# Optimization experiments

Hardware: AMD Instinct MI355X
Metric: run time of the kernel (lower is better)

Reference implementation:

```python
import jax, jax.numpy as jnp
import numpy as np

B, T, D, H, HD, F, L = 4, 2048, 768, 8, 96, 2048, 2
EPS = 1e-6


def _l2norm(x):
    return x * jax.lax.rsqrt(jnp.sum(x * x, -1, keepdims=True) + EPS)


def _layernorm(x, w, b):
    m = jnp.mean(x, -1, keepdims=True)
    v = jnp.var(x, -1, keepdims=True)
    return (x - m) * jax.lax.rsqrt(v + 1e-5) * w + b


def setup_inputs() -> dict:
    key = jax.random.key(0)
    ks = iter(jax.random.split(key, 40))
    def p(shape, scale=0.02):
        return jax.random.normal(next(ks), shape, jnp.float32) * scale
    return dict(
        hidden_states=jax.random.normal(next(ks), (B, T, D), jnp.float32),
        attention_mask=jnp.ones((B, T), jnp.float32),
        norm_a_w=jnp.ones((D,), jnp.float32), norm_a_b=jnp.zeros((D,), jnp.float32),
        proj_a_w=p((D, D)), proj_a_b=jnp.zeros((D,), jnp.float32),
        ln_w=jnp.ones((L, D), jnp.float32), ln_b=jnp.zeros((L, D), jnp.float32),
        Wq=p((L, D, H * HD)), Wk=p((L, D, H * HD)), Wv=p((L, D, H * HD)),
        Wfa=p((L, D, HD)), Wfb=p((L, HD, H * HD)),
        dt_bias=jnp.zeros((L, H * HD), jnp.float32),
        A_log=jnp.zeros((L, H * HD), jnp.float32),
        Wb=p((L, D, H)),
        Wga=p((L, D, HD)), Wgb=p((L, HD, H * HD)),
        onorm_w=jnp.ones((L, HD), jnp.float32),
        Wo=p((L, H * HD, D)),
        Wgate=p((L, D, F)), Wup=p((L, D, F)), Wdown=p((L, F, D)),
    )


def _kda_attn(x, mask, Wq, Wk, Wv, Wfa, Wfb, dt_bias, A_log, Wb, Wga, Wgb, onorm_w, Wo):
    # x: [B,T,D]; mask zeros out padded tokens
    x = x * mask[..., None]
    q = jax.nn.silu(x @ Wq).reshape(B, T, H, HD)
    k = jax.nn.silu(x @ Wk).reshape(B, T, H, HD)
    v = jax.nn.silu(x @ Wv).reshape(B, T, H, HD)
    q = _l2norm(q) * (HD ** -0.5)
    k = _l2norm(k)
    # per-channel log forget gate (negative): [B,T,H,HD]
    g = (-jnp.exp(A_log) * jax.nn.softplus((x @ Wfa) @ Wfb + dt_bias)).reshape(B, T, H, HD)
    beta = jax.nn.sigmoid(x @ Wb)  # [B,T,H]

    def step(S, qkvgb):
        qt, kt, vt, gt, bt = qkvgb  # [B,H,HD] / beta [B,H]
        S = S * jnp.exp(gt)[..., None]                      # decay along key dim
        kv = jnp.einsum('bhk,bhkv->bhv', kt, S)             # current memory read
        delta = (vt - kv) * bt[..., None]                   # delta-rule update
        S = S + jnp.einsum('bhk,bhv->bhkv', kt, delta)
        o = jnp.einsum('bhk,bhkv->bhv', qt, S)
        return S, o

    S0 = jnp.zeros((B, H, HD, HD), x.dtype)
    tm = lambda a: jnp.swapaxes(a, 0, 1)  # time-major
    S, o_t = jax.lax.scan(step, S0, (tm(q), tm(k), tm(v), tm(g), tm(beta)))
    o = jnp.swapaxes(o_t, 0, 1)  # [B,T,H,HD]
    # gated RMSNorm per head then output projection
    gate = ((x @ Wga) @ Wgb).reshape(B, T, H, HD)
    o = o * jax.lax.rsqrt(jnp.mean(o * o, -1, keepdims=True) + EPS) * onorm_w
    o = o * jax.nn.silu(gate)
    return o.reshape(B, T, H * HD) @ Wo, S


def _swiglu(x, Wgate, Wup, Wdown):
    return (jax.nn.silu(x @ Wgate) * (x @ Wup)) @ Wdown


def reference(hidden_states, attention_mask, norm_a_w, norm_a_b, proj_a_w, proj_a_b,
              ln_w, ln_b, Wq, Wk, Wv, Wfa, Wfb, dt_bias, A_log, Wb, Wga, Wgb,
              onorm_w, Wo, Wgate, Wup, Wdown):
    h = _layernorm(hidden_states, norm_a_w, norm_a_b)
    h = h @ proj_a_w + proj_a_b
    states = []
    for l in range(L):
        res = h
        hn = _layernorm(h, ln_w[l], ln_b[l])
        a, S = _kda_attn(hn, attention_mask, Wq[l], Wk[l], Wv[l], Wfa[l], Wfb[l],
                         dt_bias[l], A_log[l], Wb[l], Wga[l], Wgb[l], onorm_w[l], Wo[l])
        h = _swiglu(a, Wgate[l], Wup[l], Wdown[l]) + res
        states.append(S)
    return h, jnp.stack(states)
```

## Files before the change

kernel.cpp:

```cpp
#include <hip/hip_runtime.h>
#include <cstddef>
#include <cstdint>
#include <cmath>

constexpr int BB = 4, TT = 2048, DD = 768, HH = 8, HD = 96, FF = 2048, LL = 2;
constexpr int MM = BB * TT;
constexpr size_t HROW = (size_t)MM * DD;
constexpr int CH = 64;
constexpr int NCH = TT / CH;
constexpr int RP = 100;
constexpr int KP = 104;

typedef float f32x4 __attribute__((ext_vector_type(4)));
typedef short bf16x8 __attribute__((ext_vector_type(8)));
typedef unsigned short u16x8 __attribute__((ext_vector_type(8)));

__device__ __forceinline__ void gload16(const void* g, void* l) {
    __builtin_amdgcn_global_load_lds(
        (const __attribute__((address_space(1))) void*)g,
        (__attribute__((address_space(3))) void*)l, 16, 0, 0);
}
__device__ __forceinline__ float bf2f(unsigned short u) {
    return __uint_as_float(((unsigned)u) << 16);
}
__device__ __forceinline__ unsigned short f2bf(float f) {
    unsigned u = __float_as_uint(f);
    unsigned r = (u + 0x7fffu + ((u >> 16) & 1u)) >> 16;
    return (unsigned short)r;
}

__global__ __launch_bounds__(256)
void layernorm_rows(const float* __restrict__ x, unsigned short* __restrict__ y,
                    const float* __restrict__ w, const float* __restrict__ b,
                    const float* mask)
{
    const int row = blockIdx.x;
    const int tid = threadIdx.x;
    const float* xr = x + (size_t)row * DD;
    float v0 = xr[tid], v1 = xr[tid + 256], v2 = xr[tid + 512];
    float s = v0 + v1 + v2;
    float ss = v0 * v0 + v1 * v1 + v2 * v2;
#pragma unroll
    for (int i = 1; i < 64; i <<= 1) { s += __shfl_xor(s, i); ss += __shfl_xor(ss, i); }
    __shared__ float red[8];
    const int wid = tid >> 6, lane = tid & 63;
    if (lane == 0) { red[wid] = s; red[4 + wid] = ss; }
    __syncthreads();
    const float S  = red[0] + red[1] + red[2] + red[3];
    const float SS = red[4] + red[5] + red[6] + red[7];
    const float mean = S * (1.f / DD);
    const float var  = SS * (1.f / DD) - mean * mean;
    const float rstd = rsqrtf(var + 1e-5f);
    const float m = mask ? mask[row] : 1.f;
    unsigned short* yr = y + (size_t)row * DD;
    yr[tid]       = f2bf(((v0 - mean) * rstd * w[tid]       + b[tid])       * m);
    yr[tid + 256] = f2bf(((v1 - mean) * rstd * w[tid + 256] + b[tid + 256]) * m);
    yr[tid + 512] = f2bf(((v2 - mean) * rstd * w[tid + 512] + b[tid + 512]) * m);
}

__global__ __launch_bounds__(256)
void layernorm_rows_b(const unsigned short* __restrict__ x, unsigned short* __restrict__ y,
                      const float* __restrict__ w, const float* __restrict__ b,
                      const float* mask)
{
    const int row = blockIdx.x;
    const int tid = threadIdx.x;
    const unsigned short* xr = x + (size_t)row * DD;
    float v0 = bf2f(xr[tid]), v1 = bf2f(xr[tid + 256]), v2 = bf2f(xr[tid + 512]);
    float s = v0 + v1 + v2;
    float ss = v0 * v0 + v1 * v1 + v2 * v2;
#pragma unroll
    for (int i = 1; i < 64; i <<= 1) { s += __shfl_xor(s, i); ss += __shfl_xor(ss, i); }
    __shared__ float red[8];
    const int wid = tid >> 6, lane = tid & 63;
    if (lane == 0) { red[wid] = s; red[4 + wid] = ss; }
    __syncthreads();
    const float S  = red[0] + red[1] + red[2] + red[3];
    const float SS = red[4] + red[5] + red[6] + red[7];
    const float mean = S * (1.f / DD);
    const float var  = SS * (1.f / DD) - mean * mean;
    const float rstd = rsqrtf(var + 1e-5f);
    const float m = mask ? mask[row] : 1.f;
    unsigned short* yr = y + (size_t)row * DD;
    yr[tid]       = f2bf(((v0 - mean) * rstd * w[tid]       + b[tid])       * m);
    yr[tid + 256] = f2bf(((v1 - mean) * rstd * w[tid + 256] + b[tid + 256]) * m);
    yr[tid + 512] = f2bf(((v2 - mean) * rstd * w[tid + 512] + b[tid + 512]) * m);
}

__global__ __launch_bounds__(256)
void transcvt_all(const float* __restrict__ proj,
                  const float* __restrict__ Wq, const float* __restrict__ Wk,
                  const float* __restrict__ Wv, const float* __restrict__ Wo,
                  const float* __restrict__ Wfb, const float* __restrict__ Wgb,
                  const float* __restrict__ Wfa, const float* __restrict__ Wga,
                  const float* __restrict__ Wb, const float* __restrict__ Wgate,
                  const float* __restrict__ Wup, const float* __restrict__ Wdown,
                  unsigned short* __restrict__ wt)
{
    const int bid = blockIdx.x;
    const float* in; unsigned short* out; int K, N, sub;
    if (bid < 576) { in = proj; out = wt; K = 768; N = 768; sub = bid; }
    else {
        const int rem = bid - 576;
        const int l = rem / 7392, r = rem - l * 7392;
        unsigned short* wl = wt + 589824 + (size_t)l * 7421952;
        if (r < 2304) {
            const int j = r / 576; sub = r % 576;
            in = (j == 0 ? Wq : j == 1 ? Wk : j == 2 ? Wv : Wo) + (size_t)l * 589824;
            out = wl + (size_t)j * 589824; K = 768; N = 768;
        } else if (r < 2448) {
            const int j = (r - 2304) / 72; sub = (r - 2304) % 72;
            in = (j == 0 ? Wfb : Wgb) + (size_t)l * 73728;
            out = wl + 2359296 + (size_t)j * 73728; K = 96; N = 768;
        } else if (r < 2592) {
            const int j = (r - 2448) / 72; sub = (r - 2448) % 72;
            in = (j == 0 ? Wfa : Wga) + (size_t)l * 73728;
            out = wl + 2506752 + (size_t)j * 73728; K = 768; N = 96;
        } else if (r < 2784) {
            const int e = (r - 2592) * 256 + threadIdx.x;
            const int n = e / 768, kk = e - n * 768;
            const float* wb = Wb + (size_t)l * 6144;
            (wl + 2654208)[(size_t)n * 768 + kk] =
                (n < 8) ? f2bf(wb[(size_t)kk * 8 + n]) : (unsigned short)0;
            return;
        } else {
            const int rr = r - 2784;
            const int j = rr / 1536; sub = rr % 1536;
            if (j == 0)      { in = Wgate + (size_t)l * 1572864; out = wl + 2703360; K = 768; N = 2048; }
            else if (j == 1) { in = Wup   + (size_t)l * 1572864; out = wl + 4276224; K = 768; N = 2048; }
            else             { in = Wdown + (size_t)l * 1572864; out = wl + 5849088; K = 2048; N = 768; }
        }
    }
    __shared__ float t32[32][33];
    const int tx = threadIdx.x & 31, ty = threadIdx.x >> 5;
    const int nbx = N / 32;
    const int bx = sub % nbx, by = sub / nbx;
    const int k0 = by * 32, n0 = bx * 32;
#pragma unroll
    for (int i = 0; i < 4; ++i)
        t32[ty + i * 8][tx] = in[(size_t)(k0 + ty + i * 8) * N + n0 + tx];
    __syncthreads();
#pragma unroll
    for (int i = 0; i < 4; ++i)
        out[(size_t)(n0 + ty + i * 8) * K + k0 + tx] = f2bf(t32[tx][ty + i * 8]);
}

enum { BE_BIASB = 0, BE_BF16, BE_RESB, BE_RESF, BE_QKV };

template <int EPI, int NH>
__global__ __launch_bounds__(256)
void bgemm(const unsigned short* __restrict__ A, const unsigned short* __restrict__ Bt,
           float* Cf, unsigned short* Cb,
           const float* P0, const float* P1,
           int M, int N, int K)
{
    __shared__ unsigned short As[NH][128 * 32];
    __shared__ unsigned short Bs[NH][128 * 32];
    const int tid = threadIdx.x;
    const int w = tid >> 6, l = tid & 63;
    const int wm = w >> 1, wn = w & 1;
    const int lr = l & 15, lh = l >> 4;
    const int m0 = blockIdx.y * 128, n0 = blockIdx.x * 128;

    f32x4 acc[4][4];
#pragma unroll
    for (int i = 0; i < 4; ++i)
#pragma unroll
        for (int j = 0; j < 4; ++j) acc[i][j] = (f32x4){0.f, 0.f, 0.f, 0.f};

    const int sr = l >> 2, sq = (l & 3) * 8;
    const unsigned short* Ag = A + (size_t)(m0 + w * 32 + sr) * K + sq;
    const unsigned short* Bg = Bt + (size_t)(n0 + w * 32 + sr) * K + sq;
    const int lofs = (w * 32) * 32;

    for (int kt = 0; kt < K; kt += 32 * NH) {
        __syncthreads();
#pragma unroll
        for (int hh = 0; hh < NH; ++hh) {
            gload16(Ag + kt + hh * 32, &As[hh][lofs]);
            gload16(Ag + kt + hh * 32 + 16 * (size_t)K, &As[hh][lofs + 16 * 32]);
            gload16(Bg + kt + hh * 32, &Bs[hh][lofs]);
            gload16(Bg + kt + hh * 32 + 16 * (size_t)K, &Bs[hh][lofs + 16 * 32]);
        }
        __syncthreads();
#pragma unroll
        for (int hh = 0; hh < NH; ++hh) {
            bf16x8 af[4], bfv[4];
#pragma unroll
            for (int mi = 0; mi < 4; ++mi)
                af[mi] = *(const bf16x8*)&As[hh][(wm * 64 + mi * 16 + lr) * 32 + lh * 8];
#pragma unroll
            for (int ni = 0; ni < 4; ++ni)
                bfv[ni] = *(const bf16x8*)&Bs[hh][(wn * 64 + ni * 16 + lr) * 32 + lh * 8];
#pragma unroll
            for (int mi = 0; mi < 4; ++mi)
#pragma unroll
                for (int ni = 0; ni < 4; ++ni)
                    acc[mi][ni] = __builtin_amdgcn_mfma_f32_16x16x32_bf16(af[mi], bfv[ni], acc[mi][ni], 0, 0, 0);
        }
    }

#pragma unroll
    for (int mi = 0; mi < 4; ++mi) {
#pragma unroll
        for (int j = 0; j < 4; ++j) {
            const int row = m0 + wm * 64 + mi * 16 + lh * 4 + j;
#pragma unroll
            for (int ni = 0; ni < 4; ++ni) {
                const int col = n0 + wn * 64 + ni * 16 + lr;
                const size_t idx = (size_t)row * N + col;
                float v = acc[mi][ni][j];
                if constexpr (EPI == BE_BIASB) { Cb[idx] = f2bf(v + P0[col]); }
                else if constexpr (EPI == BE_BF16) { Cb[idx] = f2bf(v); }
                else if constexpr (EPI == BE_RESB) {
                    Cb[idx] = f2bf(v + bf2f(((const unsigned short*)P0)[idx]));
                }
                else if constexpr (EPI == BE_RESF) {
                    Cf[idx] = v + bf2f(((const unsigned short*)P0)[idx]);
                }
                else if constexpr (EPI == BE_QKV) {
                    const int tgt = col / 768;
                    const int cl = col - tgt * 768;
                    unsigned short* dst = (tgt == 0) ? Cb
                                        : (tgt == 1) ? (unsigned short*)P0
                                                     : (unsigned short*)P1;
                    dst[(size_t)row * 768 + cl] = f2bf(v / (1.f + expf(-v)));
                }
            }
        }
    }
}

__global__ __launch_bounds__(256)
void bgemm_dual(const unsigned short* __restrict__ A,
                const unsigned short* __restrict__ Bg_, const unsigned short* __restrict__ Bu_,
                unsigned short* __restrict__ C, int M, int N, int K)
{
    __shared__ unsigned short As[2][128 * 32];
    __shared__ unsigned short Bs1[2][64 * 32];
    __shared__ unsigned short Bs2[2][64 * 32];
    const int tid = threadIdx.x;
    const int w = tid >> 6, l = tid & 63;
    const int wm = w >> 1, wn = w & 1;
    const int lr = l & 15, lh = l >> 4;
    const int m0 = blockIdx.y * 128, n0 = blockIdx.x * 64;

    f32x4 a1[4][2], a2[4][2];
#pragma unroll
    for (int i = 0; i < 4; ++i)
#pragma unroll
        for (int j = 0; j < 2; ++j) { a1[i][j] = (f32x4){0.f,0.f,0.f,0.f}; a2[i][j] = (f32x4){0.f,0.f,0.f,0.f}; }

    const int sr = l >> 2, sq = (l & 3) * 8;
    const unsigned short* Ag  = A   + (size_t)(m0 + w * 32 + sr) * K + sq;
    const unsigned short* B1g = Bg_ + (size_t)(n0 + w * 16 + sr) * K + sq;
    const unsigned short* B2g = Bu_ + (size_t)(n0 + w * 16 + sr) * K + sq;
    const int aofs = (w * 32) * 32;
    const int bofs = (w * 16) * 32;

    for (int kt = 0; kt < K; kt += 64) {
        __syncthreads();
#pragma unroll
        for (int hh = 0; hh < 2; ++hh) {
            gload16(Ag + kt + hh * 32, &As[hh][aofs]);
            gload16(Ag + kt + hh * 32 + 16 * (size_t)K, &As[hh][aofs + 16 * 32]);
            gload16(B1g + kt + hh * 32, &Bs1[hh][bofs]);
            gload16(B2g + kt + hh * 32, &Bs2[hh][bofs]);
        }
        __syncthreads();
#pragma unroll
        for (int hh = 0; hh < 2; ++hh) {
            bf16x8 af[4], b1[2], b2[2];
#pragma unroll
            for (int mi = 0; mi < 4; ++mi)
                af[mi] = *(const bf16x8*)&As[hh][(wm * 64 + mi * 16 + lr) * 32 + lh * 8];
#pragma unroll
            for (int ni = 0; ni < 2; ++ni) {
                b1[ni] = *(const bf16x8*)&Bs1[hh][(wn * 32 + ni * 16 + lr) * 32 + lh * 8];
                b2[ni] = *(const bf16x8*)&Bs2[hh][(wn * 32 + ni * 16 + lr) * 32 + lh * 8];
            }
#pragma unroll
            for (int mi = 0; mi < 4; ++mi)
#pragma unroll
                for (int ni = 0; ni < 2; ++ni) {
                    a1[mi][ni] = __builtin_amdgcn_mfma_f32_16x16x32_bf16(af[mi], b1[ni], a1[mi][ni], 0, 0, 0);
                    a2[mi][ni] = __builtin_amdgcn_mfma_f32_16x16x32_bf16(af[mi], b2[ni], a2[mi][ni], 0, 0, 0);
                }
        }
    }

#pragma unroll
    for (int mi = 0; mi < 4; ++mi)
#pragma unroll
        for (int j = 0; j < 4; ++j) {
            const int row = m0 + wm * 64 + mi * 16 + lh * 4 + j;
#pragma unroll
            for (int ni = 0; ni < 2; ++ni) {
                const int col = n0 + wn * 32 + ni * 16 + lr;
                const float g = a1[mi][ni][j], u = a2[mi][ni][j];
                C[(size_t)row * N + col] = f2bf((g / (1.f + expf(-g))) * u);
            }
        }
}

__global__ __launch_bounds__(256)
void bgemm_fg(const unsigned short* __restrict__ A, const unsigned short* __restrict__ Bt,
              unsigned short* __restrict__ Cfa, unsigned short* __restrict__ Cga,
              float* __restrict__ bout, int K)
{
    __shared__ unsigned short As[2][128 * 32];
    __shared__ unsigned short Bs[2][64 * 32];
    const int tid = threadIdx.x;
    const int w = tid >> 6, l = tid & 63;
    const int wm = w >> 1, wn = w & 1;
    const int lr = l & 15, lh = l >> 4;
    const int m0 = blockIdx.y * 128, n0 = blockIdx.x * 64;

    f32x4 acc[4][2];
#pragma unroll
    for (int i = 0; i < 4; ++i)
#pragma unroll
        for (int j = 0; j < 2; ++j) acc[i][j] = (f32x4){0.f, 0.f, 0.f, 0.f};

    const int sr = l >> 2, sq = (l & 3) * 8;
    const unsigned short* Ag = A + (size_t)(m0 + w * 32 + sr) * K + sq;
    const unsigned short* Bg = Bt + (size_t)(n0 + w * 16 + sr) * K + sq;
    const int aofs = (w * 32) * 32;
    const int bofs = (w * 16) * 32;

    for (int kt = 0; kt < K; kt += 64) {
        __syncthreads();
#pragma unroll
        for (int hh = 0; hh < 2; ++hh) {
            gload16(Ag + kt + hh * 32, &As[hh][aofs]);
            gload16(Ag + kt + hh * 32 + 16 * (size_t)K, &As[hh][aofs + 16 * 32]);
            gload16(Bg + kt + hh * 32, &Bs[hh][bofs]);
        }
        __syncthreads();
#pragma unroll
        for (int hh = 0; hh < 2; ++hh) {
            bf16x8 af[4], bfv[2];
#pragma unroll
            for (int mi = 0; mi < 4; ++mi)
                af[mi] = *(const bf16x8*)&As[hh][(wm * 64 + mi * 16 + lr) * 32 + lh * 8];
#pragma unroll
            for (int ni = 0; ni < 2; ++ni)
                bfv[ni] = *(const bf16x8*)&Bs[hh][(wn * 32 + ni * 16 + lr) * 32 + lh * 8];
#pragma unroll
            for (int mi = 0; mi < 4; ++mi)
#pragma unroll
                for (int ni = 0; ni < 2; ++ni)
                    acc[mi][ni] = __builtin_amdgcn_mfma_f32_16x16x32_bf16(af[mi], bfv[ni], acc[mi][ni], 0, 0, 0);
        }
    }

#pragma unroll
    for (int mi = 0; mi < 4; ++mi)
#pragma unroll
        for (int j = 0; j < 4; ++j) {
            const int row = m0 + wm * 64 + mi * 16 + lh * 4 + j;
#pragma unroll
            for (int ni = 0; ni < 2; ++ni) {
                const int col = n0 + wn * 32 + ni * 16 + lr;
                const float v = acc[mi][ni][j];
                if (col < HD)            Cfa[(size_t)row * HD + col] = f2bf(v);
                else if (col < 2 * HD)   Cga[(size_t)row * HD + col - HD] = f2bf(v);
                else if (col < 2 * HD + HH)
                    bout[(size_t)row * HH + (col - 2 * HD)] = 1.f / (1.f + expf(-v));
            }
        }
}

constexpr int TBP = 72;
constexpr int XLP = 72;
__global__ __launch_bounds__(256)
void kda_pre(const unsigned short* __restrict__ q, const unsigned short* __restrict__ k,
             unsigned short* v,
             const unsigned short* __restrict__ fab, const float* __restrict__ Alog,
             const float* __restrict__ dtb, const unsigned short* __restrict__ wfb,
             const float* __restrict__ beta,
             unsigned short* __restrict__ ol, float* __restrict__ Bc,
             unsigned short* __restrict__ Wbf, unsigned short* __restrict__ Ktg,
             unsigned short* __restrict__ qeb)
{
    __shared__ unsigned short Kb[CH * KP];
    __shared__ float Qp[CH * RP];
    __shared__ float sb[CH];
    __shared__ float qn[CH], kn[CH];
    __shared__ __align__(16) char uR[36864];
    unsigned short* Kk   = (unsigned short*)uR;
    unsigned short* Xall = (unsigned short*)uR;
    unsigned short* Abf  = (unsigned short*)(uR + 27648);
    unsigned short* Tb   = (unsigned short*)(uR + 27648);
    unsigned short* Xl   = (unsigned short*)uR;

    const int blk = blockIdx.x;
    const int ch = blk & 31, bh = blk >> 5;
    const int b = bh >> 3, h = bh & 7;
    const int tid = threadIdx.x;
    const size_t base = (size_t)b * (TT * HH * HD) + (size_t)(ch * CH) * (HH * HD) + h * HD;
    const size_t tok0 = (size_t)b * TT + ch * CH;

    for (int e = tid; e < CH * 12; e += 256) {
        const int t = e / 12, c8 = (e % 12) * 8;
        *(u16x8*)&Kb[t * KP + c8] = *(const u16x8*)(k + base + (size_t)t * 768 + c8);
    }
    if (tid < CH) sb[tid] = beta[((size_t)b * TT + ch * CH + tid) * HH + h];

    {
        const int lane = tid & 63, w = tid >> 6;
        const int lr = lane & 15, lh = lane >> 4;
        const int t0 = w * 16;
        bf16x8 afr[3];
#pragma unroll
        for (int ks = 0; ks < 3; ++ks)
            afr[ks] = *(const bf16x8*)(fab + (tok0 + t0 + lr) * HD + ks * 32 + lh * 8);
#pragma unroll
        for (int nt = 0; nt < 6; ++nt) {
            f32x4 acc = (f32x4){0.f, 0.f, 0.f, 0.f};
#pragma unroll
            for (int ks = 0; ks < 3; ++ks) {
                const bf16x8 bfr = *(const bf16x8*)(wfb +
                    (size_t)(h * HD + nt * 16 + lr) * HD + ks * 32 + lh * 8);
                acc = __builtin_amdgcn_mfma_f32_16x16x32_bf16(afr[ks], bfr, acc, 0, 0, 0);
            }
            const int c = nt * 16 + lr;
            const float na = -expf(Alog[h * HD + c]);
            const float db = dtb[h * HD + c];
#pragma unroll
            for (int r = 0; r < 4; ++r) {
                const int t = t0 + lh * 4 + r;
                const float lin = acc[r] + db;
                const float sp = (lin > 20.f) ? lin : log1pf(expf(lin));
                Qp[t * RP + c] = na * sp;
            }
        }
    }
    __syncthreads();

    {
        const int t = tid >> 2, s = tid & 3;
        float ssq = 0.f, ssk = 0.f;
#pragma unroll
        for (int i = 0; i < 3; ++i) {
            const u16x8 qv8 = *(const u16x8*)(q + base + (size_t)t * 768 + s * 24 + i * 8);
            const u16x8 kv8 = *(const u16x8*)&Kb[t * KP + s * 24 + i * 8];
#pragma unroll
            for (int j2 = 0; j2 < 8; ++j2) {
                const float qv = bf2f(qv8[j2]);
                const float kv = bf2f(kv8[j2]);
                ssq = fmaf(qv, qv, ssq);
                ssk = fmaf(kv, kv, ssk);
            }
        }
        ssq += __shfl_xor(ssq, 1); ssq += __shfl_xor(ssq, 2);
        ssk += __shfl_xor(ssk, 1); ssk += __shfl_xor(ssk, 2);
        if (s == 0) {
            qn[t] = rsqrtf(ssq + 1e-6f) * 0.1020620726159658f;
            kn[t] = rsqrtf(ssk + 1e-6f);
        }
    }
    __syncthreads();

    if (tid < HD) {
        float L = 0.f;
        for (int t = 0; t < CH; ++t) { L += Qp[t * RP + tid]; Qp[t * RP + tid] = L; }
    }
    __syncthreads();

    for (int e = tid; e < CH * HD; e += 256) {
        const int t = e / HD, c = e % HD;
        const float L = Qp[t * RP + c];
        const float B = expf(L), iB = expf(-L);
        const float kv = bf2f(Kb[t * KP + c]) * kn[t];
        if (t == CH - 1) Bc[((size_t)bh * NCH + ch) * HD + c] = B;
        Kk[t * KP + c] = f2bf(kv * B);
        const unsigned short kti = f2bf(kv * iB);
        const float qv = bf2f(q[base + (size_t)t * 768 + c]) * qn[t];
        Kb[t * KP + c] = kti;
        Qp[t * RP + c] = qv * B;
    }
    __syncthreads();

#pragma unroll
    for (int i = 0; i < 3; ++i) {
        const int u = i * 256 + tid;
        const int c = u / 8, t8 = (u % 8) * 8;
        u16x8 vv;
#pragma unroll
        for (int j = 0; j < 8; ++j) vv[j] = Kb[(t8 + j) * KP + c];
        *(u16x8*)(Ktg + (((size_t)bh * NCH + ch) * HD + c) * CH + t8) = vv;
    }

    {
        const int lane = tid & 63;
        const int lr = lane & 15, lh = lane >> 4;
        const int t0 = (tid >> 6) * 16;
        bf16x8 afr[3];
#pragma unroll
        for (int ks = 0; ks < 3; ++ks)
            afr[ks] = *(const bf16x8*)&Kk[(t0 + lr) * KP + ks * 32 + lh * 8];
#pragma unroll
        for (int i0 = 0; i0 < 64; i0 += 16) {
            f32x4 acc = (f32x4){0.f, 0.f, 0.f, 0.f};
#pragma unroll
            for (int ks = 0; ks < 3; ++ks) {
                const bf16x8 bfr = *(const bf16x8*)&Kb[(i0 + lr) * KP + ks * 32 + lh * 8];
                acc = __builtin_amdgcn_mfma_f32_16x16x32_bf16(afr[ks], bfr, acc, 0, 0, 0);
            }
#pragma unroll
            for (int r = 0; r < 4; ++r) {
                const int t = t0 + lh * 4 + r;
                const int i = i0 + lr;
                Abf[t * 72 + i] = (i < t) ? f2bf(acc[r] * sb[t]) : (unsigned short)0;
            }
        }
    }
    __syncthreads();

    float X[CH];
    const int j = tid;
    if (j < 192) {
        if (j < HD) {
#pragma unroll
            for (int t = 0; t < CH; ++t) X[t] = sb[t] * bf2f(v[base + (size_t)t * 768 + j]);
        } else {
#pragma unroll
            for (int t = 0; t < CH; ++t) X[t] = sb[t] * bf2f(Kk[t * KP + (j - HD)]);
        }
    }
    __syncthreads();
    for (int e = tid; e < 192 * XLP; e += 256) Xall[e] = 0;
    __syncthreads();

#pragma unroll
    for (int p = 0; p < 4; ++p) {
        if (p > 0) {
            const int lane = tid & 63, w = tid >> 6;
            const int lr = lane & 15, lh = lane >> 4;
#pragma unroll
            for (int e = 0; e < 3; ++e) {
                const int col0 = (w * 3 + e) * 16;
                f32x4 uacc = (f32x4){0.f, 0.f, 0.f, 0.f};
#pragma unroll
                for (int q2 = 0; q2 < 2; ++q2) {
                    const bf16x8 aa = *(const bf16x8*)&Abf[(p * 16 + lr) * 72 + q2 * 32 + lh * 8];
                    const bf16x8 xx = *(const bf16x8*)&Xall[(col0 + lr) * XLP + q2 * 32 + lh * 8];
                    uacc = __builtin_amdgcn_mfma_f32_16x16x32_bf16(aa, xx, uacc, 0, 0, 0);
                }
#pragma unroll
                for (int r = 0; r < 4; ++r)
                    Xall[(col0 + lr) * XLP + p * 16 + lh * 4 + r] = f2bf(uacc[r]);
            }
            __syncthreads();
        }
        if (j < 192) {
            if (p > 0) {
                const u16x8 c0 = *(const u16x8*)&Xall[j * XLP + p * 16];
                const u16x8 c1 = *(const u16x8*)&Xall[j * XLP + p * 16 + 8];
#pragma unroll
                for (int rr = 0; rr < 8; ++rr) {
                    X[p * 16 + rr]     -= bf2f(c0[rr]);
                    X[p * 16 + 8 + rr] -= bf2f(c1[rr]);
                }
            }
#pragma unroll
            for (int tr = 0; tr < 16; ++tr) {
                float a = 0.f;
#pragma unroll
                for (int i = 0; i < 16; ++i)
                    if (i < tr)
                        a = fmaf(bf2f(Abf[(p * 16 + tr) * 72 + p * 16 + i]), X[p * 16 + i], a);
                X[p * 16 + tr] -= a;
            }
            u16x8 s0, s1;
#pragma unroll
            for (int rr = 0; rr < 8; ++rr) {
                s0[rr] = f2bf(X[p * 16 + rr]);
                s1[rr] = f2bf(X[p * 16 + 8 + rr]);
            }
            *(u16x8*)&Xall[j * XLP + p * 16] = s0;
            *(u16x8*)&Xall[j * XLP + p * 16 + 8] = s1;
        }
        __syncthreads();
    }

    if (j < 192) {
        if (j < HD) {
#pragma unroll
            for (int t = 0; t < CH; ++t) v[base + (size_t)t * 768 + j] = f2bf(X[t]);
        } else {
#pragma unroll
            for (int t = 0; t < CH; ++t) Wbf[base + (size_t)t * 768 + (j - HD)] = f2bf(-X[t]);
        }
    }
    __syncthreads();

    {
        const int lane = tid & 63;
        const int lr = lane & 15, lh = lane >> 4;
        const int t0 = (tid >> 6) * 16;
        bf16x8 afr[3];
#pragma unroll
        for (int ks = 0; ks < 3; ++ks) {
            const float4 qa = *(const float4*)&Qp[(t0 + lr) * RP + ks * 32 + lh * 8];
            const float4 qc = *(const float4*)&Qp[(t0 + lr) * RP + ks * 32 + lh * 8 + 4];
            bf16x8 a;
            a[0] = (short)f2bf(qa.x); a[1] = (short)f2bf(qa.y);
            a[2] = (short)f2bf(qa.z); a[3] = (short)f2bf(qa.w);
            a[4] = (short)f2bf(qc.x); a[5] = (short)f2bf(qc.y);
            a[6] = (short)f2bf(qc.z); a[7] = (short)f2bf(qc.w);
            afr[ks] = a;
        }
#pragma unroll
        for (int i0 = 0; i0 < 64; i0 += 16) {
            f32x4 acc = (f32x4){0.f, 0.f, 0.f, 0.f};
#pragma unroll
            for (int ks = 0; ks < 3; ++ks) {
                const bf16x8 bfr = *(const bf16x8*)&Kb[(i0 + lr) * KP + ks * 32 + lh * 8];
                acc = __builtin_amdgcn_mfma_f32_16x16x32_bf16(afr[ks], bfr, acc, 0, 0, 0);
            }
#pragma unroll
            for (int r = 0; r < 4; ++r) {
                const int t = t0 + lh * 4 + r;
                const int i = i0 + lr;
                Tb[t * TBP + i] = (i <= t) ? f2bf(acc[r]) : (unsigned short)0;
            }
        }
    }
    __syncthreads();

    {
        const int lane = tid & 63;
        const int lr = lane & 15, lh = lane >> 4;
        const int w = tid >> 6;
        const int t0 = w * 16;
        bf16x8 af0 = *(const bf16x8*)&Tb[(t0 + lr) * TBP + lh * 8];
        bf16x8 af1 = *(const bf16x8*)&Tb[(t0 + lr) * TBP + 32 + lh * 8];
#pragma unroll
        for (int nt = 0; nt < 12; ++nt) {
            const int n0 = nt * 16;
            f32x4 acc = (f32x4){0.f, 0.f, 0.f, 0.f};
            acc = __builtin_amdgcn_mfma_f32_16x16x32_bf16(
                af0, *(const bf16x8*)&Xl[(n0 + lr) * XLP + lh * 8], acc, 0, 0, 0);
            acc = __builtin_amdgcn_mfma_f32_16x16x32_bf16(
                af1, *(const bf16x8*)&Xl[(n0 + lr) * XLP + 32 + lh * 8], acc, 0, 0, 0);
            const int jc = n0 + lr;
#pragma unroll
            for (int r = 0; r < 4; ++r) {
                const int t = t0 + lh * 4 + r;
                if (jc < HD) ol[base + (size_t)t * 768 + jc] = f2bf(acc[r]);
                else         qeb[base + (size_t)t * 768 + (jc - HD)] = f2bf(Qp[t * RP + (jc - HD)] - acc[r]);
            }
        }
    }
}

constexpr int VSL = 16;
constexpr int WNP = 120;
constexpr int KTP2 = 72;
constexpr int DBP = 72;
constexpr int SBP = 120;
__global__ __launch_bounds__(256)
void kda_seq(const unsigned short* __restrict__ Wbf, const unsigned short* __restrict__ Ktg,
             const unsigned short* __restrict__ U, const float* __restrict__ Bc,
             unsigned short* __restrict__ SinT, float* __restrict__ states)
{
    __shared__ unsigned short Wn[CH * WNP];
    __shared__ unsigned short Kt[HD * KTP2];
    __shared__ unsigned short Dbt[VSL * DBP];
    __shared__ unsigned short Sbt[VSL * SBP];

    const int blk = blockIdx.x;
    const int bh = blk / 6, vq = blk - bh * 6;
    const int b = bh >> 3, h = bh & 7;
    const int tid = threadIdx.x;
    const int w = tid >> 6, lane = tid & 63;
    const int lr = lane & 15, lh = lane >> 4;
    const int v0 = vq * VSL;
    const size_t base = (size_t)b * (TT * HH * HD) + h * HD;
    const size_t cbase = (size_t)bh * NCH;

    const int t0 = w * 16;
    const int k1 = w * 16;
    const int k2 = (w < 2) ? (4 + w) * 16 : -1;

    f32x4 accS1 = (f32x4){0.f, 0.f, 0.f, 0.f};
    f32x4 accS2 = (f32x4){0.f, 0.f, 0.f, 0.f};

    for (int e = tid; e < VSL * SBP; e += 256) Sbt[e] = 0;

    u16x8 wpf[3], kpf[3];
    float upf[4], ucur[4];

    {
        const size_t cb = base;
#pragma unroll
        for (int i = 0; i < 3; ++i) {
            const int u = i * 256 + tid;
            const int r = u / 12, c8 = (u % 12) * 8;
            wpf[i] = *(const u16x8*)(Wbf + cb + (size_t)r * 768 + c8);
        }
        const size_t kb_ = (cbase * HD) * CH;
#pragma unroll
        for (int i = 0; i < 3; ++i) {
            const int u = i * 256 + tid;
            const int c = u / 8, t8 = (u % 8) * 8;
            kpf[i] = *(const u16x8*)(Ktg + kb_ + (size_t)c * CH + t8);
        }
#pragma unroll
        for (int r = 0; r < 4; ++r)
            ucur[r] = bf2f(U[cb + (size_t)(t0 + lh * 4 + r) * 768 + v0 + lr]);
#pragma unroll
        for (int i = 0; i < 3; ++i) {
            const int u = i * 256 + tid;
            const int r = u / 12, c8 = (u % 12) * 8;
            *(u16x8*)&Wn[r * WNP + c8] = wpf[i];
        }
#pragma unroll
        for (int i = 0; i < 3; ++i) {
            const int u = i * 256 + tid;
            const int c = u / 8, t8 = (u % 8) * 8;
            *(u16x8*)&Kt[c * KTP2 + t8] = kpf[i];
        }
    }
    __syncthreads();

    for (int ch = 0; ch < NCH; ++ch) {
        if (ch + 1 < NCH) {
            const size_t cb = base + (size_t)((ch + 1) * CH) * (HH * HD);
#pragma unroll
            for (int i = 0; i < 3; ++i) {
                const int u = i * 256 + tid;
                const int r = u / 12, c8 = (u % 12) * 8;
                wpf[i] = *(const u16x8*)(Wbf + cb + (size_t)r * 768 + c8);
            }
            const size_t kb_ = ((cbase + ch + 1) * HD) * CH;
#pragma unroll
            for (int i = 0; i < 3; ++i) {
                const int u = i * 256 + tid;
                const int c = u / 8, t8 = (u % 8) * 8;
                kpf[i] = *(const u16x8*)(Ktg + kb_ + (size_t)c * CH + t8);
            }
#pragma unroll
            for (int r = 0; r < 4; ++r)
                upf[r] = bf2f(U[cb + (size_t)(t0 + lh * 4 + r) * 768 + v0 + lr]);
        }

        if (tid < 192) {
            const int row = tid / 12, c8 = (tid % 12) * 8;
            *(u16x8*)(SinT + (size_t)(cbase + ch) * 9216 + (size_t)(v0 + row) * 96 + c8)
                = *(const u16x8*)&Sbt[row * SBP + c8];
        }

        f32x4 del = (f32x4){ucur[0], ucur[1], ucur[2], ucur[3]};
#pragma unroll
        for (int ks = 0; ks < 3; ++ks) {
            const bf16x8 a = *(const bf16x8*)&Wn[(t0 + lr) * WNP + ks * 32 + lh * 8];
            const bf16x8 bb = *(const bf16x8*)&Sbt[lr * SBP + ks * 32 + lh * 8];
            del = __builtin_amdgcn_mfma_f32_16x16x32_bf16(a, bb, del, 0, 0, 0);
        }
#pragma unroll
        for (int r = 0; r < 4; ++r)
            Dbt[lr * DBP + t0 + lh * 4 + r] = f2bf(del[r]);
        __syncthreads();

        const float* bc = Bc + (cbase + ch) * HD;
#pragma unroll
        for (int ks = 0; ks < 2; ++ks) {
            const bf16x8 a = *(const bf16x8*)&Kt[(k1 + lr) * KTP2 + ks * 32 + lh * 8];
            const bf16x8 bb = *(const bf16x8*)&Dbt[lr * DBP + ks * 32 + lh * 8];
            accS1 = __builtin_amdgcn_mfma_f32_16x16x32_bf16(a, bb, accS1, 0, 0, 0);
        }
#pragma unroll
        for (int r = 0; r < 4; ++r) accS1[r] *= bc[k1 + lh * 4 + r];
        if (k2 >= 0) {
#pragma unroll
            for (int ks = 0; ks < 2; ++ks) {
                const bf16x8 a = *(const bf16x8*)&Kt[(k2 + lr) * KTP2 + ks * 32 + lh * 8];
                const bf16x8 bb = *(const bf16x8*)&Dbt[lr * DBP + ks * 32 + lh * 8];
                accS2 = __builtin_amdgcn_mfma_f32_16x16x32_bf16(a, bb, accS2, 0, 0, 0);
            }
#pragma unroll
            for (int r = 0; r < 4; ++r) accS2[r] *= bc[k2 + lh * 4 + r];
        }
        __syncthreads();

#pragma unroll
        for (int r = 0; r < 4; ++r)
            Sbt[lr * SBP + k1 + lh * 4 + r] = f2bf(accS1[r]);
        if (k2 >= 0) {
#pragma unroll
            for (int r = 0; r < 4; ++r)
                Sbt[lr * SBP + k2 + lh * 4 + r] = f2bf(accS2[r]);
        }
        if (ch + 1 < NCH) {
#pragma unroll
            for (int i = 0; i < 3; ++i) {
                const int u = i * 256 + tid;
                const int r = u / 12, c8 = (u % 12) * 8;
                *(u16x8*)&Wn[r * WNP + c8] = wpf[i];
            }
#pragma unroll
            for (int i = 0; i < 3; ++i) {
                const int u = i * 256 + tid;
                const int c = u / 8, t8 = (u % 8) * 8;
                *(u16x8*)&Kt[c * KTP2 + t8] = kpf[i];
            }
#pragma unroll
            for (int r = 0; r < 4; ++r) ucur[r] = upf[r];
        }
        __syncthreads();
    }

    {
        float* sp = states + (size_t)bh * (HD * HD);
#pragma unroll
        for (int r = 0; r < 4; ++r)
            sp[(size_t)(k1 + lh * 4 + r) * HD + v0 + lr] = accS1[r];
        if (k2 >= 0) {
#pragma unroll
            for (int r = 0; r < 4; ++r)
                sp[(size_t)(k2 + lh * 4 + r) * HD + v0 + lr] = accS2[r];
        }
    }
}

__global__ __launch_bounds__(256)
void kda_epi(const unsigned short* __restrict__ SinT, const unsigned short* __restrict__ Qe,
             const unsigned short* __restrict__ Ol,
             const unsigned short* __restrict__ gab, const unsigned short* __restrict__ wgb,
             const float* __restrict__ onw, unsigned short* __restrict__ obf)
{
    __shared__ unsigned short Sl[96 * 104];
    __shared__ unsigned short Ql[64 * 104];
    __shared__ unsigned short Olb[64 * 104];
    __shared__ float onws[HD];

    const int bx = blockIdx.x;
    const int bh = bx >> 5, ch = bx & 31;
    const int b = bh >> 3, h = bh & 7;
    const int tid = threadIdx.x;
    const size_t cb = (size_t)b * (TT * HH * HD) + (size_t)(ch * CH) * (HH * HD) + h * HD;
    const size_t sbase = (size_t)(bh * NCH + ch) * 9216;
    const size_t tok0 = (size_t)b * TT + ch * CH;

#pragma unroll
    for (int i = 0; i < 5; ++i) {
        const int u = i * 256 + tid;
        if (u < 1152) {
            const int row = u / 12, c8 = (u % 12) * 8;
            *(u16x8*)&Sl[row * 104 + c8] = *(const u16x8*)(SinT + sbase + (size_t)row * 96 + c8);
        }
    }
#pragma unroll
    for (int i = 0; i < 3; ++i) {
        const int u = i * 256 + tid;
        const int t = u / 12, c8 = (u % 12) * 8;
        *(u16x8*)&Ql[t * 104 + c8]  = *(const u16x8*)(Qe + cb + (size_t)t * 768 + c8);
        *(u16x8*)&Olb[t * 104 + c8] = *(const u16x8*)(Ol + cb + (size_t)t * 768 + c8);
    }
    if (tid < HD) onws[tid] = onw[tid];

    const int lane = tid & 63, w = tid >> 6;
    const int lr = lane & 15, lh = lane >> 4;
    const int t0 = w * 16;

    bf16x8 gaf[3];
#pragma unroll
    for (int ks = 0; ks < 3; ++ks)
        gaf[ks] = *(const bf16x8*)(gab + (tok0 + t0 + lr) * HD + ks * 32 + lh * 8);
    f32x4 gacc[6];
#pragma unroll
    for (int nt = 0; nt < 6; ++nt) {
        gacc[nt] = (f32x4){0.f, 0.f, 0.f, 0.f};
#pragma unroll
        for (int ks = 0; ks < 3; ++ks) {
            const bf16x8 bfr = *(const bf16x8*)(wgb +
                (size_t)(h * HD + nt * 16 + lr) * HD + ks * 32 + lh * 8);
            gacc[nt] = __builtin_amdgcn_mfma_f32_16x16x32_bf16(gaf[ks], bfr, gacc[nt], 0, 0, 0);
        }
    }
    __syncthreads();

    bf16x8 af[3];
#pragma unroll
    for (int ks = 0; ks < 3; ++ks)
        af[ks] = *(const bf16x8*)&Ql[(t0 + lr) * 104 + ks * 32 + lh * 8];

    f32x4 acc[6];
#pragma unroll
    for (int nt = 0; nt < 6; ++nt) {
#pragma unroll
        for (int r = 0; r < 4; ++r)
            acc[nt][r] = bf2f(Olb[(t0 + lh * 4 + r) * 104 + nt * 16 + lr]);
#pragma unroll
        for (int ks = 0; ks < 3; ++ks)
            acc[nt] = __builtin_amdgcn_mfma_f32_16x16x32_bf16(
                af[ks], *(const bf16x8*)&Sl[(nt * 16 + lr) * 104 + ks * 32 + lh * 8],
                acc[nt], 0, 0, 0);
    }

    float ss0 = 0.f, ss1 = 0.f, ss2 = 0.f, ss3 = 0.f;
#pragma unroll
    for (int nt = 0; nt < 6; ++nt) {
        ss0 = fmaf(acc[nt][0], acc[nt][0], ss0);
        ss1 = fmaf(acc[nt][1], acc[nt][1], ss1);
        ss2 = fmaf(acc[nt][2], acc[nt][2], ss2);
        ss3 = fmaf(acc[nt][3], acc[nt][3], ss3);
    }
#pragma unroll
    for (int d = 1; d < 16; d <<= 1) {
        ss0 += __shfl_xor(ss0, d); ss1 += __shfl_xor(ss1, d);
        ss2 += __shfl_xor(ss2, d); ss3 += __shfl_xor(ss3, d);
    }
    const float rr0 = rsqrtf(ss0 * (1.f / HD) + 1e-6f);
    const float rr1 = rsqrtf(ss1 * (1.f / HD) + 1e-6f);
    const float rr2 = rsqrtf(ss2 * (1.f / HD) + 1e-6f);
    const float rr3 = rsqrtf(ss3 * (1.f / HD) + 1e-6f);

#pragma unroll
    for (int nt = 0; nt < 6; ++nt) {
        const int v = nt * 16 + lr;
        const float ow = onws[v];
#pragma unroll
        for (int r = 0; r < 4; ++r) {
            const int t = t0 + lh * 4 + r;
            const float rrv = (r == 0) ? rr0 : (r == 1) ? rr1 : (r == 2) ? rr2 : rr3;
            const float gg = gacc[nt][r];
            const float val = acc[nt][r] * rrv * ow * (gg / (1.f + expf(-gg)));
            obf[cb + (size_t)t * 768 + v] = f2bf(val);
        }
    }
}

extern "C" void kernel_launch(void* const* d_in, const int* in_sizes, int n_in,
                              void* d_out, int out_size, void* d_ws, size_t ws_size,
                              hipStream_t stream)
{
    (void)in_sizes; (void)n_in; (void)out_size; (void)ws_size;
    const float* hidden   = (const float*)d_in[0];
    const float* mask     = (const float*)d_in[1];
    const float* norm_a_w = (const float*)d_in[2];
    const float* norm_a_b = (const float*)d_in[3];
    const float* proj_a_w = (const float*)d_in[4];
    const float* proj_a_b = (const float*)d_in[5];
    const float* ln_w     = (const float*)d_in[6];
    const float* ln_b     = (const float*)d_in[7];
    const float* Wq       = (const float*)d_in[8];
    const float* Wk       = (const float*)d_in[9];
    const float* Wv       = (const float*)d_in[10];
    const float* Wfa      = (const float*)d_in[11];
    const float* Wfb      = (const float*)d_in[12];
    const float* dt_bias  = (const float*)d_in[13];
    const float* A_log    = (const float*)d_in[14];
    const float* Wb       = (const float*)d_in[15];
    const float* Wga      = (const float*)d_in[16];
    const float* Wgb      = (const float*)d_in[17];
    const float* onorm_w  = (const float*)d_in[18];
    const float* Wo       = (const float*)d_in[19];
    const float* Wgate    = (const float*)d_in[20];
    const float* Wup      = (const float*)d_in[21];
    const float* Wdown    = (const float*)d_in[22];

    float* ws    = (float*)d_ws;
    float* hbuf  = ws;
    float* qb    = ws + HROW;
    float* kb    = ws + 2 * HROW;
    float* vb    = ws + 3 * HROW;
    float* egb   = ws + 4 * HROW;
    float* betab = ws + 5 * HROW;
    float* BcP   = betab + (size_t)MM * HH;
    unsigned short* SinT = (unsigned short*)egb;
    unsigned short* hb16 = (unsigned short*)hbuf;
    unsigned short* q16 = (unsigned short*)qb;
    unsigned short* k16 = (unsigned short*)kb;
    unsigned short* v16 = (unsigned short*)vb;
    unsigned short* bfp = (unsigned short*)(BcP + 32 * NCH * HD);
    unsigned short* x_bf    = bfp;  bfp += HROW;
    unsigned short* fab_bf  = bfp;  bfp += (size_t)MM * HD;
    unsigned short* gab_bf  = bfp;  bfp += (size_t)MM * HD;
    unsigned short* olb_bf  = bfp;  bfp += HROW;
    unsigned short* w_bf    = bfp;  bfp += HROW;
    unsigned short* k_bf    = bfp;  bfp += HROW;
    unsigned short* qe_bf   = bfp;  bfp += HROW;
    unsigned short* wt_proj = bfp;  bfp += 768 * 768;
    unsigned short *wt_q[LL], *wt_fb[LL], *wt_gb[LL], *wt_fg[LL],
                   *wt_gate[LL], *wt_up[LL], *wt_down[LL], *wt_o[LL];
    for (int l = 0; l < LL; ++l) {
        wt_q[l] = bfp;    bfp += 3 * 768 * 768;
        wt_o[l] = bfp;    bfp += 768 * 768;
        wt_fb[l] = bfp;   bfp += 768 * 96;
        wt_gb[l] = bfp;   bfp += 768 * 96;
        wt_fg[l] = bfp;   bfp += 256 * 768;
        wt_gate[l] = bfp; bfp += 2048 * 768;
        wt_up[l] = bfp;   bfp += 2048 * 768;
        wt_down[l] = bfp; bfp += 768 * 2048;
    }
    unsigned short* mg_bf = (unsigned short*)qb;
    unsigned short* a_bf  = (unsigned short*)vb;

    float* out    = (float*)d_out;
    float* states = out + HROW;

    transcvt_all<<<15360, 256, 0, stream>>>(proj_a_w, Wq, Wk, Wv, Wo, Wfb, Wgb,
                                            Wfa, Wga, Wb, Wgate, Wup, Wdown, wt_proj);

    layernorm_rows<<<MM, 256, 0, stream>>>(hidden, x_bf, norm_a_w, norm_a_b, nullptr);
    bgemm<BE_BIASB, 2><<<dim3(6, 64), 256, 0, stream>>>(x_bf, wt_proj, nullptr, hb16,
                                                        proj_a_b, nullptr, MM, DD, DD);

    for (int l = 0; l < LL; ++l) {
        layernorm_rows_b<<<MM, 256, 0, stream>>>(hb16, x_bf, ln_w + l * DD, ln_b + l * DD, mask);
        bgemm<BE_QKV, 2><<<dim3(18, 64), 256, 0, stream>>>(x_bf, wt_q[l], nullptr, q16,
                                                           (const float*)k16, (const float*)v16,
                                                           MM, 3 * DD, DD);
        bgemm_fg<<<dim3(4, 64), 256, 0, stream>>>(x_bf, wt_fg[l], fab_bf, gab_bf, betab, DD);
        kda_pre<<<1024, 256, 0, stream>>>(q16, k16, v16, fab_bf, A_log + l * DD, dt_bias + l * DD,
                                          wt_fb[l], betab, olb_bf, BcP, w_bf, k_bf, qe_bf);
        kda_seq<<<192, 256, 0, stream>>>(w_bf, k_bf, v16, BcP, SinT,
                                         states + (size_t)l * BB * HH * HD * HD);
        kda_epi<<<1024, 256, 0, stream>>>(SinT, qe_bf, olb_bf, gab_bf, wt_gb[l],
                                          onorm_w + l * HD, x_bf);
        bgemm<BE_BF16, 2><<<dim3(6, 64), 256, 0, stream>>>(x_bf, wt_o[l], nullptr, a_bf, nullptr, nullptr, MM, DD, DD);
        bgemm_dual<<<dim3(32, 64), 256, 0, stream>>>(a_bf, wt_gate[l], wt_up[l], mg_bf, MM, FF, DD);
        if (l == LL - 1)
            bgemm<BE_RESF, 2><<<dim3(6, 64), 256, 0, stream>>>(mg_bf, wt_down[l], out, nullptr,
                                                               (const float*)hb16, nullptr, MM, DD, FF);
        else
            bgemm<BE_RESB, 2><<<dim3(6, 64), 256, 0, stream>>>(mg_bf, wt_down[l], nullptr, hb16,
                                                               (const float*)hb16, nullptr, MM, DD, FF);
    }
}
```

Before: 793.1 us.

## Fuse QKV and forget/gate/beta projections into one GEMM; add XCD block swizzle

Repacks the per-layer transposed weights so Wq, Wk, Wv, Wfa, Wga and Wb form one contiguous 2560-column B matrix, and replaces the separate QKV GEMM and small fa/ga/beta GEMM with a single kernel whose epilogue routes columns to the right outputs. This removes one launch and one extra pass over the normalized activations. It also adds an XCD-aware workgroup index swizzle to all GEMMs so neighbouring tiles land on the same chiplet for better L2 reuse. The cost is some wasted padded columns (2504 to 2560) and a branchier epilogue.

```diff
diff --git a/kernel.cpp b/kernel.cpp
--- a/kernel.cpp
+++ b/kernel.cpp
@@ -27,6 +27,9 @@
     unsigned u = __float_as_uint(f);
     unsigned r = (u + 0x7fffu + ((u >> 16) & 1u)) >> 16;
     return (unsigned short)r;
+}
+__device__ __forceinline__ int xcd_swz(int wg, int nwg) {
+    return (wg & 7) * (nwg >> 3) + (wg >> 3);
 }
 
 __global__ __launch_bounds__(256)
@@ -107,20 +110,21 @@
         if (r < 2304) {
             const int j = r / 576; sub = r % 576;
             in = (j == 0 ? Wq : j == 1 ? Wk : j == 2 ? Wv : Wo) + (size_t)l * 589824;
-            out = wl + (size_t)j * 589824; K = 768; N = 768;
+            out = (j < 3) ? (wl + (size_t)j * 589824) : (wl + 1966080);
+            K = 768; N = 768;
         } else if (r < 2448) {
             const int j = (r - 2304) / 72; sub = (r - 2304) % 72;
             in = (j == 0 ? Wfb : Wgb) + (size_t)l * 73728;
-            out = wl + 2359296 + (size_t)j * 73728; K = 96; N = 768;
+            out = wl + ((j == 0) ? 2555904 : 2629632); K = 96; N = 768;
         } else if (r < 2592) {
             const int j = (r - 2448) / 72; sub = (r - 2448) % 72;
             in = (j == 0 ? Wfa : Wga) + (size_t)l * 73728;
-            out = wl + 2506752 + (size_t)j * 73728; K = 768; N = 96;
+            out = wl + ((j == 0) ? 1769472 : 1843200); K = 768; N = 96;
         } else if (r < 2784) {
             const int e = (r - 2592) * 256 + threadIdx.x;
             const int n = e / 768, kk = e - n * 768;
             const float* wb = Wb + (size_t)l * 6144;
-            (wl + 2654208)[(size_t)n * 768 + kk] =
+            (wl + 1916928)[(size_t)n * 768 + kk] =
                 (n < 8) ? f2bf(wb[(size_t)kk * 8 + n]) : (unsigned short)0;
             return;
         } else {
@@ -145,7 +149,7 @@
         out[(size_t)(n0 + ty + i * 8) * K + k0 + tx] = f2bf(t32[tx][ty + i * 8]);
 }
 
-enum { BE_BIASB = 0, BE_BF16, BE_RESB, BE_RESF, BE_QKV };
+enum { BE_BIASB = 0, BE_BF16, BE_RESB, BE_RESF };
 
 template <int EPI, int NH>
 __global__ __launch_bounds__(256)
@@ -160,7 +164,9 @@
     const int w = tid >> 6, l = tid & 63;
     const int wm = w >> 1, wn = w & 1;
     const int lr = l & 15, lh = l >> 4;
-    const int m0 = blockIdx.y * 128, n0 = blockIdx.x * 128;
+    const int nwg = gridDim.x * gridDim.y;
+    const int wg = xcd_swz(blockIdx.y * gridDim.x + blockIdx.x, nwg);
+    const int m0 = (wg / gridDim.x) * 128, n0 = (wg % gridDim.x) * 128;
 
     f32x4 acc[4][4];
 #pragma unroll
@@ -218,13 +224,86 @@
                 else if constexpr (EPI == BE_RESF) {
                     Cf[idx] = v + bf2f(((const unsigned short*)P0)[idx]);
                 }
-                else if constexpr (EPI == BE_QKV) {
+            }
+        }
+    }
+}
+
+__global__ __launch_bounds__(256)
+void bgemm_qkvfg(const unsigned short* __restrict__ A, const unsigned short* __restrict__ Bt,
+                 unsigned short* __restrict__ Cq, unsigned short* __restrict__ Ck,
+                 unsigned short* __restrict__ Cv, unsigned short* __restrict__ Cfa,
+                 unsigned short* __restrict__ Cga, float* __restrict__ bout, int K)
+{
+    constexpr int N = 2560;
+    __shared__ unsigned short As[2][128 * 32];
+    __shared__ unsigned short Bs[2][128 * 32];
+    const int tid = threadIdx.x;
+    const int w = tid >> 6, l = tid & 63;
+    const int wm = w >> 1, wn = w & 1;
+    const int lr = l & 15, lh = l >> 4;
+    const int nwg = gridDim.x * gridDim.y;
+    const int wg = xcd_swz(blockIdx.y * gridDim.x + blockIdx.x, nwg);
+    const int m0 = (wg / gridDim.x) * 128, n0 = (wg % gridDim.x) * 128;
+
+    f32x4 acc[4][4];
+#pragma unroll
+    for (int i = 0; i < 4; ++i)
+#pragma unroll
+        for (int j = 0; j < 4; ++j) acc[i][j] = (f32x4){0.f, 0.f, 0.f, 0.f};
+
+    const int sr = l >> 2, sq = (l & 3) * 8;
+    const unsigned short* Ag = A + (size_t)(m0 + w * 32 + sr) * K + sq;
+    const unsigned short* Bg = Bt + (size_t)(n0 + w * 32 + sr) * K + sq;
+    const int lofs = (w * 32) * 32;
+
+    for (int kt = 0; kt < K; kt += 64) {
+        __syncthreads();
+#pragma unroll
+        for (int hh = 0; hh < 2; ++hh) {
+            gload16(Ag + kt + hh * 32, &As[hh][lofs]);
+            gload16(Ag + kt + hh * 32 + 16 * (size_t)K, &As[hh][lofs + 16 * 32]);
+            gload16(Bg + kt + hh * 32, &Bs[hh][lofs]);
+            gload16(Bg + kt + hh * 32 + 16 * (size_t)K, &Bs[hh][lofs + 16 * 32]);
+        }
+        __syncthreads();
+#pragma unroll
+        for (int hh = 0; hh < 2; ++hh) {
+            bf16x8 af[4], bfv[4];
+#pragma unroll
+            for (int mi = 0; mi < 4; ++mi)
+                af[mi] = *(const bf16x8*)&As[hh][(wm * 64 + mi * 16 + lr) * 32 + lh * 8];
+#pragma unroll
+            for (int ni = 0; ni < 4; ++ni)
+                bfv[ni] = *(const bf16x8*)&Bs[hh][(wn * 64 + ni * 16 + lr) * 32 + lh * 8];
+#pragma unroll
+            for (int mi = 0; mi < 4; ++mi)
+#pragma unroll
+                for (int ni = 0; ni < 4; ++ni)
+                    acc[mi][ni] = __builtin_amdgcn_mfma_f32_16x16x32_bf16(af[mi], bfv[ni], acc[mi][ni], 0, 0, 0);
+        }
+    }
+
+#pragma unroll
+    for (int mi = 0; mi < 4; ++mi) {
+#pragma unroll
+        for (int j = 0; j < 4; ++j) {
+            const int row = m0 + wm * 64 + mi * 16 + lh * 4 + j;
+#pragma unroll
+            for (int ni = 0; ni < 4; ++ni) {
+                const int col = n0 + wn * 64 + ni * 16 + lr;
+                const float v = acc[mi][ni][j];
+                if (col < 2304) {
                     const int tgt = col / 768;
                     const int cl = col - tgt * 768;
-                    unsigned short* dst = (tgt == 0) ? Cb
-                                        : (tgt == 1) ? (unsigned short*)P0
-                                                     : (unsigned short*)P1;
+                    unsigned short* dst = (tgt == 0) ? Cq : (tgt == 1) ? Ck : Cv;
                     dst[(size_t)row * 768 + cl] = f2bf(v / (1.f + expf(-v)));
+                } else if (col < 2400) {
+                    Cfa[(size_t)row * HD + (col - 2304)] = f2bf(v);
+                } else if (col < 2496) {
+                    Cga[(size_t)row * HD + (col - 2400)] = f2bf(v);
+                } else if (col < 2504) {
+                    bout[(size_t)row * HH + (col - 2496)] = 1.f / (1.f + expf(-v));
                 }
             }
         }
@@ -243,7 +322,9 @@
     const int w = tid >> 6, l = tid & 63;
     const int wm = w >> 1, wn = w & 1;
     const int lr = l & 15, lh = l >> 4;
-    const int m0 = blockIdx.y * 128, n0 = blockIdx.x * 64;
+    const int nwg = gridDim.x * gridDim.y;
+    const int wg = xcd_swz(blockIdx.y * gridDim.x + blockIdx.x, nwg);
+    const int m0 = (wg / gridDim.x) * 128, n0 = (wg % gridDim.x) * 64;
 
     f32x4 a1[4][2], a2[4][2];
 #pragma unroll
@@ -299,74 +380,6 @@
                 const int col = n0 + wn * 32 + ni * 16 + lr;
                 const float g = a1[mi][ni][j], u = a2[mi][ni][j];
                 C[(size_t)row * N + col] = f2bf((g / (1.f + expf(-g))) * u);
-            }
-        }
-}
-
-__global__ __launch_bounds__(256)
-void bgemm_fg(const unsigned short* __restrict__ A, const unsigned short* __restrict__ Bt,
-              unsigned short* __restrict__ Cfa, unsigned short* __restrict__ Cga,
-              float* __restrict__ bout, int K)
-{
-    __shared__ unsigned short As[2][128 * 32];
-    __shared__ unsigned short Bs[2][64 * 32];
-    const int tid = threadIdx.x;
-    const int w = tid >> 6, l = tid & 63;
-    const int wm = w >> 1, wn = w & 1;
-    const int lr = l & 15, lh = l >> 4;
-    const int m0 = blockIdx.y * 128, n0 = blockIdx.x * 64;
-
-    f32x4 acc[4][2];
-#pragma unroll
-    for (int i = 0; i < 4; ++i)
-#pragma unroll
-        for (int j = 0; j < 2; ++j) acc[i][j] = (f32x4){0.f, 0.f, 0.f, 0.f};
-
-    const int sr = l >> 2, sq = (l & 3) * 8;
-    const unsigned short* Ag = A + (size_t)(m0 + w * 32 + sr) * K + sq;
-    const unsigned short* Bg = Bt + (size_t)(n0 + w * 16 + sr) * K + sq;
-    const int aofs = (w * 32) * 32;
-    const int bofs = (w * 16) * 32;
-
-    for (int kt = 0; kt < K; kt += 64) {
-        __syncthreads();
-#pragma unroll
-        for (int hh = 0; hh < 2; ++hh) {
-            gload16(Ag + kt + hh * 32, &As[hh][aofs]);
-            gload16(Ag + kt + hh * 32 + 16 * (size_t)K, &As[hh][aofs + 16 * 32]);
-            gload16(Bg + kt + hh * 32, &Bs[hh][bofs]);
-        }
-        __syncthreads();
-#pragma unroll
-        for (int hh = 0; hh < 2; ++hh) {
-            bf16x8 af[4], bfv[2];
-#pragma unroll
-            for (int mi = 0; mi < 4; ++mi)
-                af[mi] = *(const bf16x8*)&As[hh][(wm * 64 + mi * 16 + lr) * 32 + lh * 8];
-#pragma unroll
-            for (int ni = 0; ni < 2; ++ni)
-                bfv[ni] = *(const bf16x8*)&Bs[hh][(wn * 32 + ni * 16 + lr) * 32 + lh * 8];
-#pragma unroll
-            for (int mi = 0; mi < 4; ++mi)
-#pragma unroll
-                for (int ni = 0; ni < 2; ++ni)
-                    acc[mi][ni] = __builtin_amdgcn_mfma_f32_16x16x32_bf16(af[mi], bfv[ni], acc[mi][ni], 0, 0, 0);
-        }
-    }
-
-#pragma unroll
-    for (int mi = 0; mi < 4; ++mi)
-#pragma unroll
-        for (int j = 0; j < 4; ++j) {
-            const int row = m0 + wm * 64 + mi * 16 + lh * 4 + j;
-#pragma unroll
-            for (int ni = 0; ni < 2; ++ni) {
-                const int col = n0 + wn * 32 + ni * 16 + lr;
-                const float v = acc[mi][ni][j];
-                if (col < HD)            Cfa[(size_t)row * HD + col] = f2bf(v);
-                else if (col < 2 * HD)   Cga[(size_t)row * HD + col - HD] = f2bf(v);
-                else if (col < 2 * HD + HH)
-                    bout[(size_t)row * HH + (col - 2 * HD)] = 1.f / (1.f + expf(-v));
             }
         }
 }
@@ -984,18 +997,17 @@
     unsigned short* w_bf    = bfp;  bfp += HROW;
     unsigned short* k_bf    = bfp;  bfp += HROW;
     unsigned short* qe_bf   = bfp;  bfp += HROW;
-    unsigned short* wt_proj = bfp;  bfp += 768 * 768;
-    unsigned short *wt_q[LL], *wt_fb[LL], *wt_gb[LL], *wt_fg[LL],
-                   *wt_gate[LL], *wt_up[LL], *wt_down[LL], *wt_o[LL];
+    unsigned short* wt_proj = bfp;  bfp += 589824;
+    unsigned short *wt_qkv[LL], *wt_o[LL], *wt_fb[LL], *wt_gb[LL],
+                   *wt_gate[LL], *wt_up[LL], *wt_down[LL];
     for (int l = 0; l < LL; ++l) {
-        wt_q[l] = bfp;    bfp += 3 * 768 * 768;
-        wt_o[l] = bfp;    bfp += 768 * 768;
-        wt_fb[l] = bfp;   bfp += 768 * 96;
-        wt_gb[l] = bfp;   bfp += 768 * 96;
-        wt_fg[l] = bfp;   bfp += 256 * 768;
-        wt_gate[l] = bfp; bfp += 2048 * 768;
-        wt_up[l] = bfp;   bfp += 2048 * 768;
-        wt_down[l] = bfp; bfp += 768 * 2048;
+        wt_qkv[l] = bfp;  bfp += 2560 * 768;
+        wt_o[l] = bfp;    bfp += 589824;
+        wt_fb[l] = bfp;   bfp += 73728;
+        wt_gb[l] = bfp;   bfp += 73728;
+        wt_gate[l] = bfp; bfp += 1572864;
+        wt_up[l] = bfp;   bfp += 1572864;
+        wt_down[l] = bfp; bfp += 1572864;
     }
     unsigned short* mg_bf = (unsigned short*)qb;
     unsigned short* a_bf  = (unsigned short*)vb;
@@ -1012,10 +1024,8 @@
 
     for (int l = 0; l < LL; ++l) {
         layernorm_rows_b<<<MM, 256, 0, stream>>>(hb16, x_bf, ln_w + l * DD, ln_b + l * DD, mask);
-        bgemm<BE_QKV, 2><<<dim3(18, 64), 256, 0, stream>>>(x_bf, wt_q[l], nullptr, q16,
-                                                           (const float*)k16, (const float*)v16,
-                                                           MM, 3 * DD, DD);
-        bgemm_fg<<<dim3(4, 64), 256, 0, stream>>>(x_bf, wt_fg[l], fab_bf, gab_bf, betab, DD);
+        bgemm_qkvfg<<<dim3(20, 64), 256, 0, stream>>>(x_bf, wt_qkv[l], q16, k16, v16,
+                                                      fab_bf, gab_bf, betab, DD);
         kda_pre<<<1024, 256, 0, stream>>>(q16, k16, v16, fab_bf, A_log + l * DD, dt_bias + l * DD,
                                           wt_fb[l], betab, olb_bf, BcP, w_bf, k_bf, qe_bf);
         kda_seq<<<192, 256, 0, stream>>>(w_bf, k_bf, v16, BcP, SinT,
```

Measured after the change: 765.8 us. 1.04x faster.
